# Kernel optimization log

Hardware: AMD Instinct MI355X
Metric: run time of the kernel (lower is better)

The kernel has to match this reference:

```python
import jax, jax.numpy as jnp
import numpy as np

N_NODES = 10000
N_EDGES = 640000
NF = 128      # n_features
NH = 128      # n_hidden
NT = 128      # n_targets
LN_EPS = 1e-5


def _layer_norm(h, gamma, beta):
    mu = jnp.mean(h, axis=-1, keepdims=True)
    var = jnp.var(h, axis=-1, keepdims=True)
    return (h - mu) * jax.lax.rsqrt(var + LN_EPS) * gamma + beta


def _mlp(h, W1, b1, gamma, beta, W2, b2):
    h = jax.nn.relu(h @ W1 + b1)
    h = _layer_norm(h, gamma, beta)
    return h @ W2 + b2


def setup_inputs() -> dict:
    key = jax.random.key(0)
    ks = jax.random.split(key, 12)
    s_in = 1.0 / np.sqrt(NF + NH)
    s_h = 1.0 / np.sqrt(NH)
    return {
        "x": jax.random.normal(ks[0], (N_NODES, NF), dtype=jnp.float32),
        "edge_idx": jax.random.randint(ks[1], (2, N_EDGES), 0, N_NODES, dtype=jnp.int32),
        "edge_attr": jax.random.normal(ks[2], (N_EDGES, NH), dtype=jnp.float32),
        # node_mlp_1 params
        "W1a": jax.random.normal(ks[3], (NF + NH, NH), dtype=jnp.float32) * s_in,
        "b1a": jnp.zeros((NH,), dtype=jnp.float32),
        "g1": jnp.ones((NH,), dtype=jnp.float32),
        "be1": jnp.zeros((NH,), dtype=jnp.float32),
        "W1b": jax.random.normal(ks[4], (NH, NH), dtype=jnp.float32) * s_h,
        "b1b": jnp.zeros((NH,), dtype=jnp.float32),
        # node_mlp_2 params
        "W2a": jax.random.normal(ks[5], (NF + NH, NH), dtype=jnp.float32) * s_in,
        "b2a": jnp.zeros((NH,), dtype=jnp.float32),
        "g2": jnp.ones((NH,), dtype=jnp.float32),
        "be2": jnp.zeros((NH,), dtype=jnp.float32),
        "W2b": jax.random.normal(ks[6], (NH, NT), dtype=jnp.float32) * s_h,
        "b2b": jnp.zeros((NT,), dtype=jnp.float32),
    }


def reference(x, edge_idx, edge_attr, W1a, b1a, g1, be1, W1b, b1b,
              W2a, b2a, g2, be2, W2b, b2b):
    row, col = edge_idx[0], edge_idx[1]
    # gather source-node features and run per-edge MLP
    h = jnp.concatenate([x[col], edge_attr], axis=1)        # [E, NF+NH]
    h = _mlp(h, W1a, b1a, g1, be1, W1b, b1b)                 # [E, NH]
    # scatter_mean into target nodes
    sums = jax.ops.segment_sum(h, row, num_segments=N_NODES)
    cnt = jax.ops.segment_sum(jnp.ones((h.shape[0],), h.dtype), row,
                              num_segments=N_NODES)
    agg = sums / jnp.maximum(cnt, 1.0)[:, None]              # [N, NH]
    out = jnp.concatenate([x, agg], axis=1)                  # [N, NF+NH]
    return _mlp(out, W2a, b2a, g2, be2, W2b, b2b)            # [N, NT]
```

## Files before the change

kernel.cpp:

```cpp
#include <hip/hip_runtime.h>
#include <hip/hip_bf16.h>

#define NN 10000
#define NE 640000
#define NF 128
#define NH 128
#define NT 128
#define KA 256
#define LN_EPS 1e-5f

typedef __bf16 bf16x8 __attribute__((ext_vector_type(8)));
typedef float floatx4 __attribute__((ext_vector_type(4)));
typedef float nfloat4 __attribute__((ext_vector_type(4)));

__device__ inline unsigned short f2bf(float f) {
    unsigned int u = __float_as_uint(f);
    u += 0x7FFFu + ((u >> 16) & 1u);
    return (unsigned short)(u >> 16);
}

__device__ inline bf16x8 load_frag(const unsigned short* p) {
    uint4 u = *(const uint4*)p;
    return __builtin_bit_cast(bf16x8, u);
}

__device__ inline bf16x8 cvt8(nfloat4 v0, nfloat4 v1) {
    bf16x8 r;
    r[0] = (__bf16)v0.x; r[1] = (__bf16)v0.y; r[2] = (__bf16)v0.z; r[3] = (__bf16)v0.w;
    r[4] = (__bf16)v1.x; r[5] = (__bf16)v1.y; r[6] = (__bf16)v1.z; r[7] = (__bf16)v1.w;
    return r;
}

__device__ inline void lds_fence() {
    asm volatile("s_waitcnt lgkmcnt(0)" ::: "memory");
}

__global__ __launch_bounds__(256) void conv_weights(
    const float* __restrict__ W1a, const float* __restrict__ W1b,
    const float* __restrict__ W2a, const float* __restrict__ W2b,
    unsigned short* __restrict__ wp1a, unsigned short* __restrict__ wp1b,
    unsigned short* __restrict__ wp2a, unsigned short* __restrict__ wp2b)
{
    int tid = blockIdx.x * 256 + threadIdx.x;
    const float* src;
    unsigned short* dst;
    int t, nks;
    if (tid < 4096)        { src = W1a; dst = wp1a; t = tid;         nks = 8; }
    else if (tid < 6144)   { src = W1b; dst = wp1b; t = tid - 4096;  nks = 4; }
    else if (tid < 10240)  { src = W2a; dst = wp2a; t = tid - 6144;  nks = 8; }
    else if (tid < 12288)  { src = W2b; dst = wp2b; t = tid - 10240; nks = 4; }
    else return;

    const int f = t >> 6, l = t & 63;
    const int ct = f / nks, ks = f - ct * nks;
    const int n  = ct * 16 + (l & 15);
    const int k0 = ks * 32 + (l >> 4) * 8;
    unsigned short tmp[8];
#pragma unroll
    for (int j = 0; j < 8; ++j)
        tmp[j] = f2bf(src[(k0 + j) * 128 + n]);
    *(uint4*)&dst[t * 8] = *(const uint4*)tmp;
}

__global__ __launch_bounds__(256) void hist_kernel(
    const int* __restrict__ row, int* __restrict__ hist)
{
    int e = blockIdx.x * 256 + threadIdx.x;
    if (e < NE) atomicAdd(&hist[row[e]], 1);
}

__global__ __launch_bounds__(256) void scan_kernel(
    const int* __restrict__ hist, int* __restrict__ row_start,
    int* __restrict__ cursor)
{
    __shared__ int partials[256];
    const int t = threadIdx.x;
    const int base = t * 40;
    int s = 0;
    for (int i = 0; i < 40; ++i) {
        int b = base + i;
        if (b < NN) s += hist[b];
    }
    partials[t] = s;
    __syncthreads();
    int pre = 0;
    for (int i = 0; i < t; ++i) pre += partials[i];
    int run = pre;
    for (int i = 0; i < 40; ++i) {
        int b = base + i;
        if (b < NN) {
            row_start[b] = run;
            cursor[b] = run;
            run += hist[b];
        }
    }
    if (t == 255) row_start[NN] = NE;
}

__global__ __launch_bounds__(256) void scatter_kernel(
    const int* __restrict__ row, int* __restrict__ cursor,
    int* __restrict__ perm)
{
    int e = blockIdx.x * 256 + threadIdx.x;
    if (e < NE) {
        int p = atomicAdd(&cursor[row[e]], 1);
        perm[p] = e;
    }
}

__global__ __launch_bounds__(256, 4) void edge_mlp_kernel(
    const float* __restrict__ x,
    const int* __restrict__ erow, const int* __restrict__ ecol,
    const float* __restrict__ eattr,
    const int* __restrict__ perm,
    const unsigned short* __restrict__ wp1a, const float* __restrict__ b1a,
    const float* __restrict__ g1, const float* __restrict__ be1,
    const unsigned short* __restrict__ wp1b,
    float* __restrict__ sums)
{
    __shared__ __align__(16) float smem[64 * 132];
    __shared__ int rows_s[64];

    const int wave = threadIdx.x >> 6;
    const int lane = threadIdx.x & 63;
    const int lm   = lane & 15;
    const int lq4  = lane >> 4;
    const int e0   = blockIdx.x * 64;

    if (threadIdx.x < 64)
        rows_s[threadIdx.x] = erow[perm[e0 + threadIdx.x]];

    bf16x8 bpre[8];
#pragma unroll
    for (int ks = 0; ks < 8; ++ks)
        bpre[ks] = load_frag(&wp1a[(ks * 64 + lane) * 8]);

    unsigned short* At = (unsigned short*)smem;
    {
        const int lrow = lane >> 2;
        const int lq   = lane & 3;
        const int e = perm[e0 + wave * 16 + lrow];
        const int scol = ecol[e];
        const nfloat4* xr = (const nfloat4*)(x + (size_t)scol * NF);
        const nfloat4* ar = (const nfloat4*)(eattr + (size_t)e * NH);
        unsigned short* Ar = At + (wave * 16 + lrow) * 264;
#pragma unroll
        for (int it = 0; it < 4; ++it) {
            const int g = lq + it * 4;
            nfloat4 v0 = xr[g * 2];
            nfloat4 v1 = xr[g * 2 + 1];
            *(uint4*)&Ar[g * 8] = __builtin_bit_cast(uint4, cvt8(v0, v1));
        }
#pragma unroll
        for (int it = 0; it < 4; ++it) {
            const int g = lq + it * 4;
            nfloat4 v0 = __builtin_nontemporal_load(ar + g * 2);
            nfloat4 v1 = __builtin_nontemporal_load(ar + g * 2 + 1);
            *(uint4*)&Ar[128 + g * 8] = __builtin_bit_cast(uint4, cvt8(v0, v1));
        }
    }
    lds_fence();

    unsigned short* Tw = At + wave * 16 * 264;
    bf16x8 a1[8];
#pragma unroll
    for (int ks = 0; ks < 8; ++ks)
        a1[ks] = load_frag(&Tw[lm * 264 + ks * 32 + lq4 * 8]);

    floatx4 acc1[8];
#pragma unroll
    for (int ct = 0; ct < 8; ++ct) {
        floatx4 acc = {0.f, 0.f, 0.f, 0.f};
        const unsigned short* wr = wp1a + (ct * 8 * 64 + lane) * 8;
#pragma unroll
        for (int ks = 0; ks < 8; ++ks) {
            bf16x8 b = (ct == 0) ? bpre[ks] : load_frag(wr + ks * 512);
            acc = __builtin_amdgcn_mfma_f32_16x16x32_bf16(a1[ks], b, acc, 0, 0, 0);
        }
        acc1[ct] = acc;
    }

    bf16x8 b2pre[4];
#pragma unroll
    for (int ks = 0; ks < 4; ++ks)
        b2pre[ks] = load_frag(&wp1b[(ks * 64 + lane) * 8]);

    float sum_[4] = {0, 0, 0, 0}, sq_[4] = {0, 0, 0, 0};
#pragma unroll
    for (int ct = 0; ct < 8; ++ct) {
        const float bb = b1a[ct * 16 + lm];
#pragma unroll
        for (int i = 0; i < 4; ++i) {
            float v = acc1[ct][i] + bb;
            v = fmaxf(v, 0.f);
            acc1[ct][i] = v;
            sum_[i] += v;
            sq_[i]  += v * v;
        }
    }
#pragma unroll
    for (int m = 1; m < 16; m <<= 1) {
#pragma unroll
        for (int i = 0; i < 4; ++i) {
            sum_[i] += __shfl_xor(sum_[i], m, 64);
            sq_[i]  += __shfl_xor(sq_[i],  m, 64);
        }
    }
    float mu[4], rs[4];
#pragma unroll
    for (int i = 0; i < 4; ++i) {
        mu[i] = sum_[i] * (1.f / NH);
        float var = sq_[i] * (1.f / NH) - mu[i] * mu[i];
        rs[i] = rsqrtf(var + LN_EPS);
    }

#pragma unroll
    for (int ct = 0; ct < 8; ++ct) {
        const int c = ct * 16 + lm;
        const float gg = g1[c], bb = be1[c];
#pragma unroll
        for (int i = 0; i < 4; ++i) {
            float nv = (acc1[ct][i] - mu[i]) * rs[i] * gg + bb;
            Tw[(lq4 * 4 + i) * 264 + c] = __builtin_bit_cast(unsigned short, (__bf16)nv);
        }
    }
    lds_fence();

    bf16x8 a2[4];
#pragma unroll
    for (int ks = 0; ks < 4; ++ks)
        a2[ks] = load_frag(&Tw[lm * 264 + ks * 32 + lq4 * 8]);

#pragma unroll
    for (int ct = 0; ct < 8; ++ct) {
        floatx4 acc = {0.f, 0.f, 0.f, 0.f};
        const unsigned short* wr = wp1b + (ct * 4 * 64 + lane) * 8;
#pragma unroll
        for (int ks = 0; ks < 4; ++ks) {
            bf16x8 b = (ct == 0) ? b2pre[ks] : load_frag(wr + ks * 512);
            acc = __builtin_amdgcn_mfma_f32_16x16x32_bf16(a2[ks], b, acc, 0, 0, 0);
        }
        const int c = ct * 16 + lm;
#pragma unroll
        for (int i = 0; i < 4; ++i) {
            const int r = wave * 16 + lq4 * 4 + i;
            smem[r * 132 + c] = acc[i];
        }
    }
    __syncthreads();

    {
        const int t = threadIdx.x;
        const int cc = t & 127;
        const int jb = (t >> 7) * 32;
        float a = 0.f;
        int cur = rows_s[jb];
#pragma unroll 4
        for (int j = jb; j < jb + 32; ++j) {
            a += smem[j * 132 + cc];
            int nxt = (j + 1 < jb + 32) ? rows_s[j + 1] : -1;
            if (nxt != cur) {
                atomicAdd(&sums[cur * NH + cc], a);
                a = 0.f;
                cur = nxt;
            }
        }
    }
}

__global__ __launch_bounds__(256) void node_mlp_kernel(
    const float* __restrict__ x,
    const float* __restrict__ sums, const int* __restrict__ row_start,
    const float* __restrict__ b1b,
    const unsigned short* __restrict__ wp2a, const float* __restrict__ b2a,
    const float* __restrict__ g2, const float* __restrict__ be2,
    const unsigned short* __restrict__ wp2b, const float* __restrict__ b2b,
    float* __restrict__ out)
{
    __shared__ unsigned short Atile[4][16][KA + 8];
    __shared__ unsigned short Ttile[4][16][NH + 8];

    const int wave = threadIdx.x >> 6;
    const int lane = threadIdx.x & 63;
    const int n0 = blockIdx.x * 64 + wave * 16;

    {
        const int lrow = lane >> 2;
        const int lq   = lane & 3;
        int n = n0 + lrow;
        if (n >= NN) n = NN - 1;
        const int cntn = row_start[n + 1] - row_start[n];
        const float inv  = (cntn > 0) ? (1.f / (float)cntn) : 1.f;
        const float addb = (cntn > 0) ? 1.f : 0.f;
        const float4* xr = (const float4*)(x + n * NF);
        const float4* sr = (const float4*)(sums + n * NH);
        const float4* br = (const float4*)b1b;
        unsigned short* Ar = &Atile[wave][lrow][0];
#pragma unroll
        for (int it = 0; it < 8; ++it) {
            int c4 = lq + it * 4;
            float4 v = xr[c4];
            uint2 w;
            w.x = (unsigned)f2bf(v.x) | ((unsigned)f2bf(v.y) << 16);
            w.y = (unsigned)f2bf(v.z) | ((unsigned)f2bf(v.w) << 16);
            *(uint2*)&Ar[c4 * 4] = w;
            float4 v2 = sr[c4];
            float4 bv = br[c4];
            float a0 = v2.x * inv + addb * bv.x;
            float a1 = v2.y * inv + addb * bv.y;
            float a2 = v2.z * inv + addb * bv.z;
            float a3 = v2.w * inv + addb * bv.w;
            uint2 w2;
            w2.x = (unsigned)f2bf(a0) | ((unsigned)f2bf(a1) << 16);
            w2.y = (unsigned)f2bf(a2) | ((unsigned)f2bf(a3) << 16);
            *(uint2*)&Ar[128 + c4 * 4] = w2;
        }
    }
    __syncthreads();

    const int lm  = lane & 15;
    const int lq4 = lane >> 4;

    bf16x8 a1[8];
#pragma unroll
    for (int ks = 0; ks < 8; ++ks)
        a1[ks] = load_frag(&Atile[wave][lm][ks * 32 + lq4 * 8]);

    floatx4 acc1[8];
#pragma unroll
    for (int ct = 0; ct < 8; ++ct) {
        floatx4 acc = {0.f, 0.f, 0.f, 0.f};
        const unsigned short* wr = wp2a + (ct * 8 * 64 + lane) * 8;
#pragma unroll
        for (int ks = 0; ks < 8; ++ks) {
            bf16x8 b = load_frag(wr + ks * 512);
            acc = __builtin_amdgcn_mfma_f32_16x16x32_bf16(a1[ks], b, acc, 0, 0, 0);
        }
        acc1[ct] = acc;
    }

    float sum_[4] = {0, 0, 0, 0}, sq_[4] = {0, 0, 0, 0};
#pragma unroll
    for (int ct = 0; ct < 8; ++ct) {
        const float bb = b2a[ct * 16 + lm];
#pragma unroll
        for (int i = 0; i < 4; ++i) {
            float v = acc1[ct][i] + bb;
            v = fmaxf(v, 0.f);
            acc1[ct][i] = v;
            sum_[i] += v;
            sq_[i]  += v * v;
        }
    }
#pragma unroll
    for (int m = 1; m < 16; m <<= 1) {
#pragma unroll
        for (int i = 0; i < 4; ++i) {
            sum_[i] += __shfl_xor(sum_[i], m, 64);
            sq_[i]  += __shfl_xor(sq_[i],  m, 64);
        }
    }
    float mu[4], rs[4];
#pragma unroll
    for (int i = 0; i < 4; ++i) {
        mu[i] = sum_[i] * (1.f / NH);
        float var = sq_[i] * (1.f / NH) - mu[i] * mu[i];
        rs[i] = rsqrtf(var + LN_EPS);
    }
#pragma unroll
    for (int ct = 0; ct < 8; ++ct) {
        const int c = ct * 16 + lm;
        const float gg = g2[c], bb = be2[c];
#pragma unroll
        for (int i = 0; i < 4; ++i) {
            float nv = (acc1[ct][i] - mu[i]) * rs[i] * gg + bb;
            Ttile[wave][lq4 * 4 + i][c] = f2bf(nv);
        }
    }
    __syncthreads();

    bf16x8 a2[4];
#pragma unroll
    for (int ks = 0; ks < 4; ++ks)
        a2[ks] = load_frag(&Ttile[wave][lm][ks * 32 + lq4 * 8]);

#pragma unroll
    for (int ct = 0; ct < 8; ++ct) {
        floatx4 acc = {0.f, 0.f, 0.f, 0.f};
        const unsigned short* wr = wp2b + (ct * 4 * 64 + lane) * 8;
#pragma unroll
        for (int ks = 0; ks < 4; ++ks) {
            bf16x8 b = load_frag(wr + ks * 512);
            acc = __builtin_amdgcn_mfma_f32_16x16x32_bf16(a2[ks], b, acc, 0, 0, 0);
        }
        const int c = ct * 16 + lm;
        const float bb = b2b[c];
#pragma unroll
        for (int i = 0; i < 4; ++i) {
            int n = n0 + lq4 * 4 + i;
            if (n < NN) out[n * NT + c] = acc[i] + bb;
        }
    }
}

extern "C" void kernel_launch(void* const* d_in, const int* in_sizes, int n_in,
                              void* d_out, int out_size, void* d_ws, size_t ws_size,
                              hipStream_t stream) {
    const float* x     = (const float*)d_in[0];
    const int*   eidx  = (const int*)d_in[1];
    const float* eattr = (const float*)d_in[2];
    const float* W1a = (const float*)d_in[3];
    const float* b1a = (const float*)d_in[4];
    const float* g1  = (const float*)d_in[5];
    const float* be1 = (const float*)d_in[6];
    const float* W1b = (const float*)d_in[7];
    const float* b1b = (const float*)d_in[8];
    const float* W2a = (const float*)d_in[9];
    const float* b2a = (const float*)d_in[10];
    const float* g2  = (const float*)d_in[11];
    const float* be2 = (const float*)d_in[12];
    const float* W2b = (const float*)d_in[13];
    const float* b2b = (const float*)d_in[14];

    char* ws = (char*)d_ws;
    float* sums     = (float*)ws;
    int*   hist     = (int*)(ws + 5120000);
    int*   cursor   = (int*)(ws + 5160000);
    int*   row_start= (int*)(ws + 5200000);
    int*   perm     = (int*)(ws + 5240064);
    unsigned short* wp1a = (unsigned short*)(ws + 7800064);
    unsigned short* wp1b = (unsigned short*)(ws + 7865600);
    unsigned short* wp2a = (unsigned short*)(ws + 7898368);
    unsigned short* wp2b = (unsigned short*)(ws + 7963904);

    const int* erow = eidx;
    const int* ecol = eidx + NE;

    (void)hipMemsetAsync(ws, 0, 5160000, stream);
    conv_weights<<<48, 256, 0, stream>>>(W1a, W1b, W2a, W2b, wp1a, wp1b, wp2a, wp2b);
    hist_kernel<<<(NE + 255) / 256, 256, 0, stream>>>(erow, hist);
    scan_kernel<<<1, 256, 0, stream>>>(hist, row_start, cursor);
    scatter_kernel<<<(NE + 255) / 256, 256, 0, stream>>>(erow, cursor, perm);
    edge_mlp_kernel<<<NE / 64, 256, 0, stream>>>(x, erow, ecol, eattr, perm,
                                                 wp1a, b1a, g1, be1, wp1b, sums);
    node_mlp_kernel<<<(NN + 63) / 64, 256, 0, stream>>>(x, sums, row_start, b1b,
                                                        wp2a, b2a, g2, be2, wp2b, b2b,
                                                        (float*)d_out);
}
```

Measured before the change: 733.0 us.

## Make edge MLP persistent with register prefetch of next tile, pre-convert x to bf16

The edge MLP kernel now runs a fixed grid of 715 blocks, each looping over 14 tiles of 64 edges. The next tile's edge_attr rows and gathered x rows are loaded into registers while the current tile's MFMAs run, which aims to hide gather latency. x is converted to bf16 once in a merged prep kernel, halving the bytes of the random gather. In exchange, occupancy drops to 3 waves per SIMD, register pressure rises, and the weight fragments are no longer kept preloaded in registers.

```diff
diff --git a/kernel.cpp b/kernel.cpp
--- a/kernel.cpp
+++ b/kernel.cpp
@@ -8,6 +8,8 @@
 #define NT 128
 #define KA 256
 #define LN_EPS 1e-5f
+#define TPB 14
+#define NBE 715
 
 typedef __bf16 bf16x8 __attribute__((ext_vector_type(8)));
 typedef float floatx4 __attribute__((ext_vector_type(4)));
@@ -33,33 +35,41 @@
 
 __device__ inline void lds_fence() {
     asm volatile("s_waitcnt lgkmcnt(0)" ::: "memory");
-}
-
-__global__ __launch_bounds__(256) void conv_weights(
+    __builtin_amdgcn_sched_barrier(0);
+}
+
+__global__ __launch_bounds__(256) void prep_kernel(
+    const float* __restrict__ x,
     const float* __restrict__ W1a, const float* __restrict__ W1b,
     const float* __restrict__ W2a, const float* __restrict__ W2b,
     unsigned short* __restrict__ wp1a, unsigned short* __restrict__ wp1b,
-    unsigned short* __restrict__ wp2a, unsigned short* __restrict__ wp2b)
-{
-    int tid = blockIdx.x * 256 + threadIdx.x;
-    const float* src;
-    unsigned short* dst;
-    int t, nks;
-    if (tid < 4096)        { src = W1a; dst = wp1a; t = tid;         nks = 8; }
-    else if (tid < 6144)   { src = W1b; dst = wp1b; t = tid - 4096;  nks = 4; }
-    else if (tid < 10240)  { src = W2a; dst = wp2a; t = tid - 6144;  nks = 8; }
-    else if (tid < 12288)  { src = W2b; dst = wp2b; t = tid - 10240; nks = 4; }
-    else return;
-
-    const int f = t >> 6, l = t & 63;
-    const int ct = f / nks, ks = f - ct * nks;
-    const int n  = ct * 16 + (l & 15);
-    const int k0 = ks * 32 + (l >> 4) * 8;
-    unsigned short tmp[8];
-#pragma unroll
-    for (int j = 0; j < 8; ++j)
-        tmp[j] = f2bf(src[(k0 + j) * 128 + n]);
-    *(uint4*)&dst[t * 8] = *(const uint4*)tmp;
+    unsigned short* __restrict__ wp2a, unsigned short* __restrict__ wp2b,
+    unsigned short* __restrict__ xbf)
+{
+    const int tid = blockIdx.x * 256 + threadIdx.x;
+    const int nth = gridDim.x * 256;
+
+    const nfloat4* xs = (const nfloat4*)x;
+    uint4* xd = (uint4*)xbf;
+    for (int i = tid; i < 160000; i += nth)
+        xd[i] = __builtin_bit_cast(uint4, cvt8(xs[2 * i], xs[2 * i + 1]));
+
+    if (tid < 12288) {
+        const float* src; unsigned short* dst; int t, nks;
+        if (tid < 4096)       { src = W1a; dst = wp1a; t = tid;         nks = 8; }
+        else if (tid < 6144)  { src = W1b; dst = wp1b; t = tid - 4096;  nks = 4; }
+        else if (tid < 10240) { src = W2a; dst = wp2a; t = tid - 6144;  nks = 8; }
+        else                  { src = W2b; dst = wp2b; t = tid - 10240; nks = 4; }
+        const int f = t >> 6, l = t & 63;
+        const int ct = f / nks, ks = f - ct * nks;
+        const int n  = ct * 16 + (l & 15);
+        const int k0 = ks * 32 + (l >> 4) * 8;
+        unsigned short tmp[8];
+#pragma unroll
+        for (int j = 0; j < 8; ++j)
+            tmp[j] = f2bf(src[(k0 + j) * 128 + n]);
+        *(uint4*)&dst[t * 8] = *(const uint4*)tmp;
+    }
 }
 
 __global__ __launch_bounds__(256) void hist_kernel(
@@ -108,8 +118,8 @@
     }
 }
 
-__global__ __launch_bounds__(256, 4) void edge_mlp_kernel(
-    const float* __restrict__ x,
+__global__ __launch_bounds__(256, 3) void edge_mlp_kernel(
+    const unsigned short* __restrict__ xbf,
     const int* __restrict__ erow, const int* __restrict__ ecol,
     const float* __restrict__ eattr,
     const int* __restrict__ perm,
@@ -125,146 +135,169 @@
     const int lane = threadIdx.x & 63;
     const int lm   = lane & 15;
     const int lq4  = lane >> 4;
-    const int e0   = blockIdx.x * 64;
-
-    if (threadIdx.x < 64)
-        rows_s[threadIdx.x] = erow[perm[e0 + threadIdx.x]];
-
-    bf16x8 bpre[8];
-#pragma unroll
-    for (int ks = 0; ks < 8; ++ks)
-        bpre[ks] = load_frag(&wp1a[(ks * 64 + lane) * 8]);
+    const int lrow = lane >> 2;
+    const int lq   = lane & 3;
 
     unsigned short* At = (unsigned short*)smem;
+    unsigned short* Tw = At + wave * 16 * 264;
+
+    const int base = blockIdx.x * TPB;
+
+    int ecur = perm[base * 64 + wave * 16 + lrow];
+    nfloat4 pe[8];
+    uint4 px[4];
     {
-        const int lrow = lane >> 2;
-        const int lq   = lane & 3;
-        const int e = perm[e0 + wave * 16 + lrow];
-        const int scol = ecol[e];
-        const nfloat4* xr = (const nfloat4*)(x + (size_t)scol * NF);
-        const nfloat4* ar = (const nfloat4*)(eattr + (size_t)e * NH);
-        unsigned short* Ar = At + (wave * 16 + lrow) * 264;
-#pragma unroll
-        for (int it = 0; it < 4; ++it) {
-            const int g = lq + it * 4;
-            nfloat4 v0 = xr[g * 2];
-            nfloat4 v1 = xr[g * 2 + 1];
-            *(uint4*)&Ar[g * 8] = __builtin_bit_cast(uint4, cvt8(v0, v1));
-        }
-#pragma unroll
-        for (int it = 0; it < 4; ++it) {
-            const int g = lq + it * 4;
-            nfloat4 v0 = __builtin_nontemporal_load(ar + g * 2);
-            nfloat4 v1 = __builtin_nontemporal_load(ar + g * 2 + 1);
-            *(uint4*)&Ar[128 + g * 8] = __builtin_bit_cast(uint4, cvt8(v0, v1));
-        }
-    }
-    lds_fence();
-
-    unsigned short* Tw = At + wave * 16 * 264;
-    bf16x8 a1[8];
-#pragma unroll
-    for (int ks = 0; ks < 8; ++ks)
-        a1[ks] = load_frag(&Tw[lm * 264 + ks * 32 + lq4 * 8]);
-
-    floatx4 acc1[8];
-#pragma unroll
-    for (int ct = 0; ct < 8; ++ct) {
-        floatx4 acc = {0.f, 0.f, 0.f, 0.f};
-        const unsigned short* wr = wp1a + (ct * 8 * 64 + lane) * 8;
-#pragma unroll
-        for (int ks = 0; ks < 8; ++ks) {
-            bf16x8 b = (ct == 0) ? bpre[ks] : load_frag(wr + ks * 512);
-            acc = __builtin_amdgcn_mfma_f32_16x16x32_bf16(a1[ks], b, acc, 0, 0, 0);
-        }
-        acc1[ct] = acc;
-    }
-
-    bf16x8 b2pre[4];
-#pragma unroll
-    for (int ks = 0; ks < 4; ++ks)
-        b2pre[ks] = load_frag(&wp1b[(ks * 64 + lane) * 8]);
-
-    float sum_[4] = {0, 0, 0, 0}, sq_[4] = {0, 0, 0, 0};
-#pragma unroll
-    for (int ct = 0; ct < 8; ++ct) {
-        const float bb = b1a[ct * 16 + lm];
+        const nfloat4* ar = (const nfloat4*)(eattr + (size_t)ecur * NH);
+#pragma unroll
+        for (int t = 0; t < 4; ++t) {
+            const int g = lq + t * 4;
+            pe[2 * t]     = __builtin_nontemporal_load(ar + g * 2);
+            pe[2 * t + 1] = __builtin_nontemporal_load(ar + g * 2 + 1);
+        }
+        const uint4* xr = (const uint4*)(xbf + (size_t)ecol[ecur] * NF);
+#pragma unroll
+        for (int t = 0; t < 4; ++t)
+            px[t] = xr[lq + t * 4];
+    }
+
+    for (int it = 0; it < TPB; ++it) {
+        const int tile = base + it;
+        if (tile >= NE / 64) break;
+        const bool hasnext = (it + 1 < TPB) && (tile + 1 < NE / 64);
+
+        if (threadIdx.x < 64)
+            rows_s[threadIdx.x] = erow[perm[tile * 64 + threadIdx.x]];
+
+        {
+            unsigned short* Ar = At + (wave * 16 + lrow) * 264;
+#pragma unroll
+            for (int t = 0; t < 4; ++t)
+                *(uint4*)&Ar[(lq + t * 4) * 8] = px[t];
+#pragma unroll
+            for (int t = 0; t < 4; ++t)
+                *(uint4*)&Ar[128 + (lq + t * 4) * 8] =
+                    __builtin_bit_cast(uint4, cvt8(pe[2 * t], pe[2 * t + 1]));
+        }
+        lds_fence();
+
+        bf16x8 a1[8];
+#pragma unroll
+        for (int ks = 0; ks < 8; ++ks)
+            a1[ks] = load_frag(&At[(wave * 16 + lm) * 264 + ks * 32 + lq4 * 8]);
+
+        if (hasnext) {
+            ecur = perm[(tile + 1) * 64 + wave * 16 + lrow];
+            const nfloat4* ar = (const nfloat4*)(eattr + (size_t)ecur * NH);
+#pragma unroll
+            for (int t = 0; t < 4; ++t) {
+                const int g = lq + t * 4;
+                pe[2 * t]     = __builtin_nontemporal_load(ar + g * 2);
+                pe[2 * t + 1] = __builtin_nontemporal_load(ar + g * 2 + 1);
+            }
+        }
+
+        floatx4 acc1[8];
+#pragma unroll
+        for (int ct = 0; ct < 8; ++ct) {
+            floatx4 acc = {0.f, 0.f, 0.f, 0.f};
+            const unsigned short* wr = wp1a + (ct * 8 * 64 + lane) * 8;
+#pragma unroll
+            for (int ks = 0; ks < 8; ++ks) {
+                bf16x8 b = load_frag(wr + ks * 512);
+                acc = __builtin_amdgcn_mfma_f32_16x16x32_bf16(a1[ks], b, acc, 0, 0, 0);
+            }
+            acc1[ct] = acc;
+        }
+
+        if (hasnext) {
+            const uint4* xr = (const uint4*)(xbf + (size_t)ecol[ecur] * NF);
+#pragma unroll
+            for (int t = 0; t < 4; ++t)
+                px[t] = xr[lq + t * 4];
+        }
+
+        float sum_[4] = {0, 0, 0, 0}, sq_[4] = {0, 0, 0, 0};
+#pragma unroll
+        for (int ct = 0; ct < 8; ++ct) {
+            const float bb = b1a[ct * 16 + lm];
+#pragma unroll
+            for (int i = 0; i < 4; ++i) {
+                float v = acc1[ct][i] + bb;
+                v = fmaxf(v, 0.f);
+                acc1[ct][i] = v;
+                sum_[i] += v;
+                sq_[i]  += v * v;
+            }
+        }
+#pragma unroll
+        for (int m = 1; m < 16; m <<= 1) {
+#pragma unroll
+            for (int i = 0; i < 4; ++i) {
+                sum_[i] += __shfl_xor(sum_[i], m, 64);
+                sq_[i]  += __shfl_xor(sq_[i],  m, 64);
+            }
+        }
+        float mu[4], rs[4];
 #pragma unroll
         for (int i = 0; i < 4; ++i) {
-            float v = acc1[ct][i] + bb;
-            v = fmaxf(v, 0.f);
-            acc1[ct][i] = v;
-            sum_[i] += v;
-            sq_[i]  += v * v;
-        }
-    }
-#pragma unroll
-    for (int m = 1; m < 16; m <<= 1) {
-#pragma unroll
-        for (int i = 0; i < 4; ++i) {
-            sum_[i] += __shfl_xor(sum_[i], m, 64);
-            sq_[i]  += __shfl_xor(sq_[i],  m, 64);
-        }
-    }
-    float mu[4], rs[4];
-#pragma unroll
-    for (int i = 0; i < 4; ++i) {
-        mu[i] = sum_[i] * (1.f / NH);
-        float var = sq_[i] * (1.f / NH) - mu[i] * mu[i];
-        rs[i] = rsqrtf(var + LN_EPS);
-    }
-
-#pragma unroll
-    for (int ct = 0; ct < 8; ++ct) {
-        const int c = ct * 16 + lm;
-        const float gg = g1[c], bb = be1[c];
-#pragma unroll
-        for (int i = 0; i < 4; ++i) {
-            float nv = (acc1[ct][i] - mu[i]) * rs[i] * gg + bb;
-            Tw[(lq4 * 4 + i) * 264 + c] = __builtin_bit_cast(unsigned short, (__bf16)nv);
-        }
-    }
-    lds_fence();
-
-    bf16x8 a2[4];
-#pragma unroll
-    for (int ks = 0; ks < 4; ++ks)
-        a2[ks] = load_frag(&Tw[lm * 264 + ks * 32 + lq4 * 8]);
-
-#pragma unroll
-    for (int ct = 0; ct < 8; ++ct) {
-        floatx4 acc = {0.f, 0.f, 0.f, 0.f};
-        const unsigned short* wr = wp1b + (ct * 4 * 64 + lane) * 8;
-#pragma unroll
-        for (int ks = 0; ks < 4; ++ks) {
-            bf16x8 b = (ct == 0) ? b2pre[ks] : load_frag(wr + ks * 512);
-            acc = __builtin_amdgcn_mfma_f32_16x16x32_bf16(a2[ks], b, acc, 0, 0, 0);
-        }
-        const int c = ct * 16 + lm;
-#pragma unroll
-        for (int i = 0; i < 4; ++i) {
-            const int r = wave * 16 + lq4 * 4 + i;
-            smem[r * 132 + c] = acc[i];
-        }
-    }
-    __syncthreads();
-
-    {
-        const int t = threadIdx.x;
-        const int cc = t & 127;
-        const int jb = (t >> 7) * 32;
-        float a = 0.f;
-        int cur = rows_s[jb];
+            mu[i] = sum_[i] * (1.f / NH);
+            float var = sq_[i] * (1.f / NH) - mu[i] * mu[i];
+            rs[i] = rsqrtf(var + LN_EPS);
+        }
+
+#pragma unroll
+        for (int ct = 0; ct < 8; ++ct) {
+            const int c = ct * 16 + lm;
+            const float gg = g1[c], bb = be1[c];
+#pragma unroll
+            for (int i = 0; i < 4; ++i) {
+                float nv = (acc1[ct][i] - mu[i]) * rs[i] * gg + bb;
+                Tw[(lq4 * 4 + i) * 264 + c] = __builtin_bit_cast(unsigned short, (__bf16)nv);
+            }
+        }
+        lds_fence();
+
+        bf16x8 a2[4];
+#pragma unroll
+        for (int ks = 0; ks < 4; ++ks)
+            a2[ks] = load_frag(&Tw[lm * 264 + ks * 32 + lq4 * 8]);
+
+#pragma unroll
+        for (int ct = 0; ct < 8; ++ct) {
+            floatx4 acc = {0.f, 0.f, 0.f, 0.f};
+            const unsigned short* wr = wp1b + (ct * 4 * 64 + lane) * 8;
+#pragma unroll
+            for (int ks = 0; ks < 4; ++ks) {
+                bf16x8 b = load_frag(wr + ks * 512);
+                acc = __builtin_amdgcn_mfma_f32_16x16x32_bf16(a2[ks], b, acc, 0, 0, 0);
+            }
+            const int c = ct * 16 + lm;
+#pragma unroll
+            for (int i = 0; i < 4; ++i) {
+                const int r = wave * 16 + lq4 * 4 + i;
+                smem[r * 132 + c] = acc[i];
+            }
+        }
+        __syncthreads();
+
+        {
+            const int t = threadIdx.x;
+            const int cc = t & 127;
+            const int jb = (t >> 7) * 32;
+            float a = 0.f;
+            int cur = rows_s[jb];
 #pragma unroll 4
-        for (int j = jb; j < jb + 32; ++j) {
-            a += smem[j * 132 + cc];
-            int nxt = (j + 1 < jb + 32) ? rows_s[j + 1] : -1;
-            if (nxt != cur) {
-                atomicAdd(&sums[cur * NH + cc], a);
-                a = 0.f;
-                cur = nxt;
-            }
-        }
+            for (int j = jb; j < jb + 32; ++j) {
+                a += smem[j * 132 + cc];
+                int nxt = (j + 1 < jb + 32) ? rows_s[j + 1] : -1;
+                if (nxt != cur) {
+                    atomicAdd(&sums[cur * NH + cc], a);
+                    a = 0.f;
+                    cur = nxt;
+                }
+            }
+        }
+        __syncthreads();
     }
 }
 
@@ -423,26 +456,28 @@
     const float* b2b = (const float*)d_in[14];
 
     char* ws = (char*)d_ws;
-    float* sums     = (float*)ws;
-    int*   hist     = (int*)(ws + 5120000);
-    int*   cursor   = (int*)(ws + 5160000);
-    int*   row_start= (int*)(ws + 5200000);
-    int*   perm     = (int*)(ws + 5240064);
+    float* sums      = (float*)ws;
+    int*   hist      = (int*)(ws + 5120000);
+    int*   cursor    = (int*)(ws + 5160000);
+    int*   row_start = (int*)(ws + 5200000);
+    int*   perm      = (int*)(ws + 5240064);
     unsigned short* wp1a = (unsigned short*)(ws + 7800064);
     unsigned short* wp1b = (unsigned short*)(ws + 7865600);
     unsigned short* wp2a = (unsigned short*)(ws + 7898368);
     unsigned short* wp2b = (unsigned short*)(ws + 7963904);
+    unsigned short* xbf  = (unsigned short*)(ws + 7996672);
 
     const int* erow = eidx;
     const int* ecol = eidx + NE;
 
     (void)hipMemsetAsync(ws, 0, 5160000, stream);
-    conv_weights<<<48, 256, 0, stream>>>(W1a, W1b, W2a, W2b, wp1a, wp1b, wp2a, wp2b);
+    prep_kernel<<<640, 256, 0, stream>>>(x, W1a, W1b, W2a, W2b,
+                                         wp1a, wp1b, wp2a, wp2b, xbf);
     hist_kernel<<<(NE + 255) / 256, 256, 0, stream>>>(erow, hist);
     scan_kernel<<<1, 256, 0, stream>>>(hist, row_start, cursor);
     scatter_kernel<<<(NE + 255) / 256, 256, 0, stream>>>(erow, cursor, perm);
-    edge_mlp_kernel<<<NE / 64, 256, 0, stream>>>(x, erow, ecol, eattr, perm,
-                                                 wp1a, b1a, g1, be1, wp1b, sums);
+    edge_mlp_kernel<<<NBE, 256, 0, stream>>>(xbf, erow, ecol, eattr, perm,
+                                             wp1a, b1a, g1, be1, wp1b, sums);
     node_mlp_kernel<<<(NN + 63) / 64, 256, 0, stream>>>(x, sums, row_start, b1b,
                                                         wp2a, b2a, g2, be2, wp2b, b2b,
                                                         (float*)d_out);
```

Result: slower. 1.063 ms (+45.0%).
